# Performance work log

Measured on AMD Instinct MI355X. Metric: run time of the kernel, lower is better.

Reference implementation:

```python
import jax, jax.numpy as jnp
import numpy as np

E = 8       # num_experts
C = 1024    # output_dim (== input_dim, so no input_proj)


def setup_inputs() -> dict:
    key = jax.random.key(0)
    ks = jax.random.split(key, 8)
    B, N = 4, 2048
    s = 0.02
    return {
        "x":    jax.random.normal(ks[0], (B, N, C), jnp.float32),
        "x_ir": jax.random.normal(ks[1], (B, N, C), jnp.float32),
        # expert Linear weights, torch layout (out, in) per expert -> (E, C, C)
        "We": jax.random.normal(ks[2], (E, C, C), jnp.float32) * s,
        "be": jax.random.normal(ks[3], (E, C), jnp.float32) * s,
        # gate: Linear(C, C//2) -> ReLU -> Linear(C//2, E)
        "gw1": jax.random.normal(ks[4], (C // 2, C), jnp.float32) * s,
        "gb1": jax.random.normal(ks[5], (C // 2,), jnp.float32) * s,
        "gw2": jax.random.normal(ks[6], (E, C // 2), jnp.float32) * s,
        "gb2": jax.random.normal(ks[7], (E,), jnp.float32) * s,
    }


def _gates(x, gw1, gb1, gw2, gb2):
    gx = x.mean(axis=1)                                   # [B, C]
    h = jax.nn.relu(gx @ gw1.T + gb1)                     # [B, C//2]
    return jax.nn.softmax(h @ gw2.T + gb2, axis=-1)       # [B, E]


def _moe(x, We, be, g):
    # Equivalent to sum_e g[b,e] * (x @ We[e].T + be[e]); since experts are
    # linear, fold gates into a per-batch weight matrix (compute-efficient).
    Wb = jnp.einsum("be,eoc->boc", g, We)                 # [B, O, C]
    bb = g @ be                                           # [B, O]
    return jnp.einsum("bnc,boc->bno", x, Wb) + bb[:, None, :]


def reference(x, x_ir, We, be, gw1, gb1, gw2, gb2):
    g = _gates(x, gw1, gb1, gw2, gb2)                     # gates computed from x only
    moe_x = _moe(x, We, be, g)
    moe_x_ir = _moe(x_ir, We, be, g)
    return (moe_x, moe_x_ir)
```

## Files before the change

kernel.cpp:

```cpp
#include <hip/hip_runtime.h>
#include <hip/hip_bf16.h>
#include <stdint.h>

#define B_  4
#define N_  2048
#define C_  1024
#define E_  8
#define H_  512

typedef __bf16 bf16x8 __attribute__((ext_vector_type(8)));
typedef __bf16 bf16x4 __attribute__((ext_vector_type(4)));
typedef float  f32x4  __attribute__((ext_vector_type(4)));

#define WB_OFF   0ull
#define PM_OFF   0ull
#define XB_OFF   (8ull*1024*1024)
#define GX_OFF   (XB_OFF + 32ull*1024*1024)
#define BB_OFF   (GX_OFF + 16384ull)
#define H_OFF    (BB_OFF + 16384ull)

__device__ __forceinline__ void gload16(const void* g, void* l) {
  __builtin_amdgcn_global_load_lds((const __attribute__((address_space(1))) void*)g,
                                   (__attribute__((address_space(3))) void*)l, 16, 0, 0);
}

#define CFENCE() asm volatile("" ::: "memory")

__global__ __launch_bounds__(256) void castmean_kernel(const float* __restrict__ x,
    const float* __restrict__ x_ir, __bf16* __restrict__ dst, float* __restrict__ pmean) {
  __shared__ float red[128][9];
  int bi = blockIdx.x;
  int half = bi >> 10, rblk = bi & 1023;
  const float* src = half ? x_ir : x;
  int t = threadIdx.x;
  int cg = t & 127, rg = t >> 7;
  int r0 = rblk * 8 + rg * 4;
  const float4* sp = (const float4*)(src + (size_t)r0 * C_) + cg * 2;
  __bf16* dp = dst + (size_t)half * ((size_t)B_ * N_ * C_) + (size_t)r0 * C_ + cg * 8;
  float s[8] = {};
  #pragma unroll
  for (int rr = 0; rr < 4; ++rr) {
    float4 a = sp[0], b4 = sp[1];
    bf16x8 o;
    o[0] = (__bf16)a.x; o[1] = (__bf16)a.y; o[2] = (__bf16)a.z; o[3] = (__bf16)a.w;
    o[4] = (__bf16)b4.x; o[5] = (__bf16)b4.y; o[6] = (__bf16)b4.z; o[7] = (__bf16)b4.w;
    *(bf16x8*)dp = o;
    s[0] += a.x; s[1] += a.y; s[2] += a.z; s[3] += a.w;
    s[4] += b4.x; s[5] += b4.y; s[6] += b4.z; s[7] += b4.w;
    sp += C_ / 4; dp += C_;
  }
  if (half == 0) {
    if (rg == 1) {
      #pragma unroll
      for (int j = 0; j < 8; ++j) red[cg][j] = s[j];
    }
    __syncthreads();
    if (rg == 0) {
      float4 lo, hi;
      lo.x = s[0] + red[cg][0]; lo.y = s[1] + red[cg][1];
      lo.z = s[2] + red[cg][2]; lo.w = s[3] + red[cg][3];
      hi.x = s[4] + red[cg][4]; hi.y = s[5] + red[cg][5];
      hi.z = s[6] + red[cg][6]; hi.w = s[7] + red[cg][7];
      float* pr = pmean + (size_t)rblk * C_ + cg * 8;
      *(float4*)pr = lo;
      *(float4*)(pr + 4) = hi;
    }
  }
}

__global__ __launch_bounds__(256) void mean2_kernel(const float* __restrict__ pmean,
                                                    float* __restrict__ gx) {
  __shared__ float red[128];
  int cs = blockIdx.x, b = blockIdx.y;
  int t = threadIdx.x;
  int c = cs * 128 + (t & 127), rh = t >> 7;
  const float* p = pmean + ((size_t)b * 256 + rh * 128) * C_ + c;
  float s = 0.f;
  #pragma unroll 8
  for (int j = 0; j < 128; ++j) s += p[(size_t)j * C_];
  if (rh == 1) red[t & 127] = s;
  __syncthreads();
  if (rh == 0) gx[b * C_ + c] = (s + red[t & 127]) * (1.0f / N_);
}

__global__ __launch_bounds__(256) void h_kernel(const float* __restrict__ gx,
    const float* __restrict__ gw1, const float* __restrict__ gb1, float* __restrict__ h) {
  __shared__ float sgx[B_][C_];
  int t = threadIdx.x;
  for (int i = t; i < B_ * C_; i += 256) sgx[i >> 10][i & 1023] = gx[i];
  __syncthreads();
  int jl = t >> 4, l16 = t & 15, b = l16 & 3, qt = l16 >> 2;
  int j = blockIdx.x * 16 + jl;
  const float4* row = (const float4*)(gw1 + (size_t)j * C_) + qt * 64;
  const float* gbase = &sgx[b][qt * 256];
  float acc = 0.f;
  #pragma unroll 8
  for (int c4 = 0; c4 < 64; ++c4) {
    float4 w = row[c4];
    acc += w.x * gbase[c4*4+0] + w.y * gbase[c4*4+1]
         + w.z * gbase[c4*4+2] + w.w * gbase[c4*4+3];
  }
  acc += __shfl_down(acc, 4, 16);
  acc += __shfl_down(acc, 8, 16);
  if (qt == 0) h[b * H_ + j] = fmaxf(acc + gb1[j], 0.f);
}

__global__ __launch_bounds__(256) void wbgate_kernel(const float* __restrict__ h,
    const float* __restrict__ gw2, const float* __restrict__ gb2,
    const float* __restrict__ be, const float* __restrict__ We,
    __bf16* __restrict__ Wb, float* __restrict__ bbp) {
  __shared__ float slog[B_ * E_];
  __shared__ float sg[B_ * E_];
  int t = threadIdx.x;
  int p = t >> 3, sub = t & 7;
  int pb = p >> 3, pe = p & 7;
  float s = 0.f;
  for (int k = sub; k < H_; k += 8) s += h[pb * H_ + k] * gw2[pe * H_ + k];
  s += __shfl_down(s, 4, 8);
  s += __shfl_down(s, 2, 8);
  s += __shfl_down(s, 1, 8);
  if (sub == 0) slog[p] = s + gb2[pe];
  __syncthreads();
  if (t < B_) {
    float m = -1e30f;
    for (int e = 0; e < E_; ++e) m = fmaxf(m, slog[t * E_ + e]);
    float pr[E_], sum = 0.f;
    for (int e = 0; e < E_; ++e) { pr[e] = __expf(slog[t * E_ + e] - m); sum += pr[e]; }
    float inv = 1.f / sum;
    for (int e = 0; e < E_; ++e) sg[t * E_ + e] = pr[e] * inv;
  }
  __syncthreads();

  int bi = blockIdx.x;
  size_t oc4 = (size_t)bi * 256 + t;
  const float4* src = (const float4*)We + oc4;
  float4 w[E_];
  #pragma unroll
  for (int e = 0; e < E_; ++e) w[e] = src[(size_t)e * (C_ * C_ / 4)];
  #pragma unroll
  for (int b = 0; b < B_; ++b) {
    float4 acc = make_float4(0.f, 0.f, 0.f, 0.f);
    #pragma unroll
    for (int e = 0; e < E_; ++e) {
      float g = sg[b * E_ + e];
      acc.x += g * w[e].x; acc.y += g * w[e].y;
      acc.z += g * w[e].z; acc.w += g * w[e].w;
    }
    bf16x4 o;
    o[0] = (__bf16)acc.x; o[1] = (__bf16)acc.y;
    o[2] = (__bf16)acc.z; o[3] = (__bf16)acc.w;
    *(bf16x4*)(Wb + ((size_t)b << 20) + oc4 * 4) = o;
  }

  if (bi < 16) {
    int ii = bi * 256 + t;
    int bb_ = ii >> 10, oo = ii & 1023;
    float sbb = 0.f;
    #pragma unroll
    for (int e = 0; e < E_; ++e) sbb += sg[bb_ * E_ + e] * be[e * C_ + oo];
    bbp[ii] = sbb;
  }
}

#define NT 16

__global__ __launch_bounds__(512, 2) void moe_gemm(const __bf16* __restrict__ Xb,
    const __bf16* __restrict__ Wb, const float* __restrict__ bb, float* __restrict__ out) {
  __shared__ __attribute__((aligned(128))) char smem[2][65536];

  const int t = threadIdx.x;
  const int wid = t >> 6, lane = t & 63;
  const int wm = wid >> 2, wn = wid & 3;

  int f = blockIdx.x;
  int swz = (f & 7) * 32 + (f >> 3);
  int xb_ = swz & 3, yb_ = (swz >> 2) & 7, z = swz >> 5;
  int b = z & 3;
  const size_t mat = (size_t)N_ * C_;
  const __bf16* A  = Xb + (size_t)z * mat;
  const __bf16* Bm = Wb + (size_t)b * C_ * C_;
  float* O = out + (size_t)z * mat;
  const int row0 = yb_ * 256, col0 = xb_ * 256;

  const int lrow8 = lane >> 3;
  const int kblk  = ((lane & 7) ^ lrow8) << 3;

  const int lr = lane & 15;
  const int swzk0 = (((lane >> 4) + 0) ^ (lane & 7)) << 4;
  const int swzk1 = (((lane >> 4) + 4) ^ (lane & 7)) << 4;

  auto stage = [&](int sid, int k0, char* buf) {
    #pragma unroll
    for (int j = 0; j < 2; ++j) {
      int u = wid * 2 + j;
      int rl0 = u * 8;
      if (sid == 0 || sid == 3) {
        int hh = (sid == 3) ? 1 : 0;
        int row_u = rl0 + (rl0 & 64) + hh * 64;
        const __bf16* src = A + (size_t)(row0 + row_u + lrow8) * C_ + k0 + kblk;
        gload16(src, buf + row_u * 128);
      } else {
        int hh = (sid == 2) ? 1 : 0;
        int col_u = (rl0 & 31) + (rl0 >> 5) * 64 + hh * 32;
        const __bf16* src = Bm + (size_t)(col0 + col_u + lrow8) * C_ + k0 + kblk;
        gload16(src, buf + 32768 + col_u * 128);
      }
    }
  };

  f32x4 acc[8][4] = {};
  bf16x8 av[2][4][2];
  bf16x8 bv[2][2][2];

  #define RD_A(buf_, Aq_, mq_) { \
    int rby = (wm * 128 + (Aq_) * 64 + (mq_) * 16 + lr) * 128; \
    av[buf_][mq_][0] = *(const bf16x8*)(rbA + rby + swzk0); \
    av[buf_][mq_][1] = *(const bf16x8*)(rbA + rby + swzk1); }
  #define RD_B(Bq_, nq_) { \
    int cby = (wn * 64 + (Bq_) * 32 + (nq_) * 16 + lr) * 128; \
    bv[Bq_][nq_][0] = *(const bf16x8*)(rbB + cby + swzk0); \
    bv[Bq_][nq_][1] = *(const bf16x8*)(rbB + cby + swzk1); }
  #define MFMA1(ab_, mq_, Bq_, nq_) { \
    acc[(ab_)*4+(mq_)][(Bq_)*2+(nq_)] = __builtin_amdgcn_mfma_f32_16x16x32_bf16( \
        av[ab_][mq_][0], bv[Bq_][nq_][0], acc[(ab_)*4+(mq_)][(Bq_)*2+(nq_)], 0, 0, 0); \
    acc[(ab_)*4+(mq_)][(Bq_)*2+(nq_)] = __builtin_amdgcn_mfma_f32_16x16x32_bf16( \
        av[ab_][mq_][1], bv[Bq_][nq_][1], acc[(ab_)*4+(mq_)][(Bq_)*2+(nq_)], 0, 0, 0); }

  #pragma unroll
  for (int sid = 0; sid < 4; ++sid) stage(sid, 0, smem[0]);
  asm volatile("s_waitcnt vmcnt(2)" ::: "memory");
  __builtin_amdgcn_s_barrier();
  CFENCE();

  for (int kt = 0; kt < NT; ++kt) {
    const char* rbA = smem[kt & 1];
    const char* rbB = rbA + 32768;
    char* wbuf = smem[(kt + 1) & 1];
    const bool more = (kt + 1 < NT);
    const int knext = (kt + 1) * 64;

    if (more) { stage(0, knext, wbuf); stage(1, knext, wbuf); }
    RD_A(0, 0, 0) RD_B(0, 0) RD_A(0, 0, 1) RD_B(0, 1) RD_A(0, 0, 2) RD_A(0, 0, 3)
    __builtin_amdgcn_s_setprio(1);
    MFMA1(0, 0, 0, 0) MFMA1(0, 0, 0, 1)
    RD_B(1, 0) RD_B(1, 1)
    MFMA1(0, 1, 0, 0) MFMA1(0, 1, 0, 1)
    MFMA1(0, 2, 0, 0) MFMA1(0, 2, 0, 1)
    MFMA1(0, 3, 0, 0) MFMA1(0, 3, 0, 1)
    __builtin_amdgcn_s_setprio(0);
    if (more) asm volatile("s_waitcnt vmcnt(4)" ::: "memory");
    else      asm volatile("s_waitcnt vmcnt(0)" ::: "memory");
    __builtin_amdgcn_s_barrier();
    CFENCE();

    if (more) { stage(2, knext, wbuf); stage(3, knext, wbuf); }
    __builtin_amdgcn_s_setprio(1);
    MFMA1(0, 0, 1, 0) MFMA1(0, 0, 1, 1)
    RD_A(1, 1, 0) RD_A(1, 1, 1)
    MFMA1(0, 1, 1, 0) MFMA1(0, 1, 1, 1)
    RD_A(1, 1, 2) RD_A(1, 1, 3)
    MFMA1(0, 2, 1, 0) MFMA1(0, 2, 1, 1)
    MFMA1(0, 3, 1, 0) MFMA1(0, 3, 1, 1)
    __builtin_amdgcn_s_setprio(0);
    __builtin_amdgcn_s_barrier();
    CFENCE();

    __builtin_amdgcn_s_setprio(1);
    MFMA1(1, 0, 0, 0) MFMA1(1, 0, 0, 1) MFMA1(1, 1, 0, 0) MFMA1(1, 1, 0, 1)
    MFMA1(1, 2, 0, 0) MFMA1(1, 2, 0, 1) MFMA1(1, 3, 0, 0) MFMA1(1, 3, 0, 1)
    MFMA1(1, 0, 1, 0) MFMA1(1, 0, 1, 1) MFMA1(1, 1, 1, 0) MFMA1(1, 1, 1, 1)
    MFMA1(1, 2, 1, 0) MFMA1(1, 2, 1, 1) MFMA1(1, 3, 1, 0) MFMA1(1, 3, 1, 1)
    __builtin_amdgcn_s_setprio(0);
    if (more) asm volatile("s_waitcnt vmcnt(2)" ::: "memory");
    __builtin_amdgcn_s_barrier();
    CFENCE();
  }

  const int er = lane >> 4;
  const f32x4 bias4 = *(const f32x4*)(bb + b * C_ + col0 + wn * 64 + lr * 4);

  #pragma unroll
  for (int m = 0; m < 8; ++m) {
    float* eb = (float*)(smem[m & 1]) + wid * (16 * 68);
    #pragma unroll
    for (int n = 0; n < 4; ++n) {
      f32x4 v = acc[m][n];
      #pragma unroll
      for (int r = 0; r < 4; ++r)
        eb[(er * 4 + r) * 68 + n * 16 + lr] = v[r];
    }
    asm volatile("s_waitcnt lgkmcnt(0)" ::: "memory");
    __builtin_amdgcn_sched_barrier(0);
    #pragma unroll
    for (int j = 0; j < 4; ++j) {
      int row = j * 4 + er;
      f32x4 v = *(const f32x4*)(eb + row * 68 + lr * 4);
      v[0] += bias4[0]; v[1] += bias4[1]; v[2] += bias4[2]; v[3] += bias4[3];
      int grow = row0 + wm * 128 + m * 16 + row;
      int gcol = col0 + wn * 64 + lr * 4;
      __builtin_nontemporal_store(v, (f32x4*)(O + (size_t)grow * C_ + gcol));
    }
  }
}

extern "C" void kernel_launch(void* const* d_in, const int* in_sizes, int n_in,
                              void* d_out, int out_size, void* d_ws, size_t ws_size,
                              hipStream_t stream) {
  const float* x    = (const float*)d_in[0];
  const float* x_ir = (const float*)d_in[1];
  const float* We   = (const float*)d_in[2];
  const float* be   = (const float*)d_in[3];
  const float* gw1  = (const float*)d_in[4];
  const float* gb1  = (const float*)d_in[5];
  const float* gw2  = (const float*)d_in[6];
  const float* gb2  = (const float*)d_in[7];
  float* out = (float*)d_out;

  char* ws = (char*)d_ws;
  __bf16* Wb    = (__bf16*)(ws + WB_OFF);
  float*  pmean = (float*)(ws + PM_OFF);
  __bf16* Xb    = (__bf16*)(ws + XB_OFF);
  float*  gx    = (float*)(ws + GX_OFF);
  float*  bbp   = (float*)(ws + BB_OFF);
  float*  h     = (float*)(ws + H_OFF);

  castmean_kernel<<<2048, 256, 0, stream>>>(x, x_ir, Xb, pmean);
  mean2_kernel<<<dim3(8, 4), 256, 0, stream>>>(pmean, gx);
  h_kernel<<<32, 256, 0, stream>>>(gx, gw1, gb1, h);
  wbgate_kernel<<<1024, 256, 0, stream>>>(h, gw2, gb2, be, We, Wb, bbp);

  moe_gemm<<<256, 512, 0, stream>>>(Xb, Wb, bbp, out);
}
```

Before: 92.13 us.

## Prefetch next k-tile LDS fragments during last MFMA phase; nontemporal loads in cast

The GEMM main loop is restructured so the A/B register fragments for the next k-tile are read from LDS during the final MFMA phase of the current tile, after the barrier that makes the next buffer visible. A prologue loads the first tile's fragments before the loop. This aims to hide LDS read latency behind MFMA issue at the start of each iteration. The cast/mean kernel also switches its fp32 input reads to nontemporal loads to reduce cache pollution. The reordering raises register pressure and depends on the barrier and waitcnt placement staying correct for the double buffer.

```diff
diff --git a/kernel.cpp b/kernel.cpp
--- a/kernel.cpp
+++ b/kernel.cpp
@@ -35,18 +35,19 @@
   int t = threadIdx.x;
   int cg = t & 127, rg = t >> 7;
   int r0 = rblk * 8 + rg * 4;
-  const float4* sp = (const float4*)(src + (size_t)r0 * C_) + cg * 2;
+  const f32x4* sp = (const f32x4*)(src + (size_t)r0 * C_) + cg * 2;
   __bf16* dp = dst + (size_t)half * ((size_t)B_ * N_ * C_) + (size_t)r0 * C_ + cg * 8;
   float s[8] = {};
   #pragma unroll
   for (int rr = 0; rr < 4; ++rr) {
-    float4 a = sp[0], b4 = sp[1];
+    f32x4 a  = __builtin_nontemporal_load(sp);
+    f32x4 b4 = __builtin_nontemporal_load(sp + 1);
     bf16x8 o;
-    o[0] = (__bf16)a.x; o[1] = (__bf16)a.y; o[2] = (__bf16)a.z; o[3] = (__bf16)a.w;
-    o[4] = (__bf16)b4.x; o[5] = (__bf16)b4.y; o[6] = (__bf16)b4.z; o[7] = (__bf16)b4.w;
+    o[0] = (__bf16)a[0]; o[1] = (__bf16)a[1]; o[2] = (__bf16)a[2]; o[3] = (__bf16)a[3];
+    o[4] = (__bf16)b4[0]; o[5] = (__bf16)b4[1]; o[6] = (__bf16)b4[2]; o[7] = (__bf16)b4[3];
     *(bf16x8*)dp = o;
-    s[0] += a.x; s[1] += a.y; s[2] += a.z; s[3] += a.w;
-    s[4] += b4.x; s[5] += b4.y; s[6] += b4.z; s[7] += b4.w;
+    s[0] += a[0]; s[1] += a[1]; s[2] += a[2]; s[3] += a[3];
+    s[4] += b4[0]; s[5] += b4[1]; s[6] += b4[2]; s[7] += b4[3];
     sp += C_ / 4; dp += C_;
   }
   if (half == 0) {
@@ -212,41 +213,43 @@
   bf16x8 av[2][4][2];
   bf16x8 bv[2][2][2];
 
-  #define RD_A(buf_, Aq_, mq_) { \
+  #define RD_A(base_, slot_, Aq_, mq_) { \
+    const char* _pA = (base_); \
     int rby = (wm * 128 + (Aq_) * 64 + (mq_) * 16 + lr) * 128; \
-    av[buf_][mq_][0] = *(const bf16x8*)(rbA + rby + swzk0); \
-    av[buf_][mq_][1] = *(const bf16x8*)(rbA + rby + swzk1); }
-  #define RD_B(Bq_, nq_) { \
+    av[slot_][mq_][0] = *(const bf16x8*)(_pA + rby + swzk0); \
+    av[slot_][mq_][1] = *(const bf16x8*)(_pA + rby + swzk1); }
+  #define RD_B(base_, Bq_, nq_) { \
+    const char* _pB = (base_) + 32768; \
     int cby = (wn * 64 + (Bq_) * 32 + (nq_) * 16 + lr) * 128; \
-    bv[Bq_][nq_][0] = *(const bf16x8*)(rbB + cby + swzk0); \
-    bv[Bq_][nq_][1] = *(const bf16x8*)(rbB + cby + swzk1); }
-  #define MFMA1(ab_, mq_, Bq_, nq_) { \
-    acc[(ab_)*4+(mq_)][(Bq_)*2+(nq_)] = __builtin_amdgcn_mfma_f32_16x16x32_bf16( \
-        av[ab_][mq_][0], bv[Bq_][nq_][0], acc[(ab_)*4+(mq_)][(Bq_)*2+(nq_)], 0, 0, 0); \
-    acc[(ab_)*4+(mq_)][(Bq_)*2+(nq_)] = __builtin_amdgcn_mfma_f32_16x16x32_bf16( \
-        av[ab_][mq_][1], bv[Bq_][nq_][1], acc[(ab_)*4+(mq_)][(Bq_)*2+(nq_)], 0, 0, 0); }
+    bv[Bq_][nq_][0] = *(const bf16x8*)(_pB + cby + swzk0); \
+    bv[Bq_][nq_][1] = *(const bf16x8*)(_pB + cby + swzk1); }
+  #define MFMA1(slot_, mq_, Bq_, nq_) { \
+    acc[(slot_)*4+(mq_)][(Bq_)*2+(nq_)] = __builtin_amdgcn_mfma_f32_16x16x32_bf16( \
+        av[slot_][mq_][0], bv[Bq_][nq_][0], acc[(slot_)*4+(mq_)][(Bq_)*2+(nq_)], 0, 0, 0); \
+    acc[(slot_)*4+(mq_)][(Bq_)*2+(nq_)] = __builtin_amdgcn_mfma_f32_16x16x32_bf16( \
+        av[slot_][mq_][1], bv[Bq_][nq_][1], acc[(slot_)*4+(mq_)][(Bq_)*2+(nq_)], 0, 0, 0); }
 
   #pragma unroll
   for (int sid = 0; sid < 4; ++sid) stage(sid, 0, smem[0]);
   asm volatile("s_waitcnt vmcnt(2)" ::: "memory");
   __builtin_amdgcn_s_barrier();
   CFENCE();
+  {
+    const char* rb0 = smem[0];
+    RD_A(rb0, 0, 0, 0) RD_A(rb0, 0, 0, 1) RD_A(rb0, 0, 0, 2) RD_A(rb0, 0, 0, 3)
+    RD_B(rb0, 0, 0) RD_B(rb0, 0, 1) RD_B(rb0, 1, 0) RD_B(rb0, 1, 1)
+  }
 
   for (int kt = 0; kt < NT; ++kt) {
     const char* rbA = smem[kt & 1];
-    const char* rbB = rbA + 32768;
     char* wbuf = smem[(kt + 1) & 1];
     const bool more = (kt + 1 < NT);
     const int knext = (kt + 1) * 64;
 
     if (more) { stage(0, knext, wbuf); stage(1, knext, wbuf); }
-    RD_A(0, 0, 0) RD_B(0, 0) RD_A(0, 0, 1) RD_B(0, 1) RD_A(0, 0, 2) RD_A(0, 0, 3)
     __builtin_amdgcn_s_setprio(1);
-    MFMA1(0, 0, 0, 0) MFMA1(0, 0, 0, 1)
-    RD_B(1, 0) RD_B(1, 1)
-    MFMA1(0, 1, 0, 0) MFMA1(0, 1, 0, 1)
-    MFMA1(0, 2, 0, 0) MFMA1(0, 2, 0, 1)
-    MFMA1(0, 3, 0, 0) MFMA1(0, 3, 0, 1)
+    MFMA1(0, 0, 0, 0) MFMA1(0, 0, 0, 1) MFMA1(0, 1, 0, 0) MFMA1(0, 1, 0, 1)
+    MFMA1(0, 2, 0, 0) MFMA1(0, 2, 0, 1) MFMA1(0, 3, 0, 0) MFMA1(0, 3, 0, 1)
     __builtin_amdgcn_s_setprio(0);
     if (more) asm volatile("s_waitcnt vmcnt(4)" ::: "memory");
     else      asm volatile("s_waitcnt vmcnt(0)" ::: "memory");
@@ -256,24 +259,29 @@
     if (more) { stage(2, knext, wbuf); stage(3, knext, wbuf); }
     __builtin_amdgcn_s_setprio(1);
     MFMA1(0, 0, 1, 0) MFMA1(0, 0, 1, 1)
-    RD_A(1, 1, 0) RD_A(1, 1, 1)
+    RD_A(rbA, 1, 1, 0) RD_A(rbA, 1, 1, 1)
     MFMA1(0, 1, 1, 0) MFMA1(0, 1, 1, 1)
-    RD_A(1, 1, 2) RD_A(1, 1, 3)
+    RD_A(rbA, 1, 1, 2) RD_A(rbA, 1, 1, 3)
     MFMA1(0, 2, 1, 0) MFMA1(0, 2, 1, 1)
     MFMA1(0, 3, 1, 0) MFMA1(0, 3, 1, 1)
     __builtin_amdgcn_s_setprio(0);
     __builtin_amdgcn_s_barrier();
     CFENCE();
 
-    __builtin_amdgcn_s_setprio(1);
-    MFMA1(1, 0, 0, 0) MFMA1(1, 0, 0, 1) MFMA1(1, 1, 0, 0) MFMA1(1, 1, 0, 1)
-    MFMA1(1, 2, 0, 0) MFMA1(1, 2, 0, 1) MFMA1(1, 3, 0, 0) MFMA1(1, 3, 0, 1)
-    MFMA1(1, 0, 1, 0) MFMA1(1, 0, 1, 1) MFMA1(1, 1, 1, 0) MFMA1(1, 1, 1, 1)
-    MFMA1(1, 2, 1, 0) MFMA1(1, 2, 1, 1) MFMA1(1, 3, 1, 0) MFMA1(1, 3, 1, 1)
-    __builtin_amdgcn_s_setprio(0);
     if (more) asm volatile("s_waitcnt vmcnt(2)" ::: "memory");
     __builtin_amdgcn_s_barrier();
     CFENCE();
+    if (more) { RD_A(wbuf, 0, 0, 0) RD_A(wbuf, 0, 0, 1) RD_A(wbuf, 0, 0, 2) RD_A(wbuf, 0, 0, 3) }
+    __builtin_amdgcn_s_setprio(1);
+    MFMA1(1, 0, 0, 0) MFMA1(1, 1, 0, 0) MFMA1(1, 2, 0, 0) MFMA1(1, 3, 0, 0)
+    MFMA1(1, 0, 0, 1) MFMA1(1, 1, 0, 1) MFMA1(1, 2, 0, 1) MFMA1(1, 3, 0, 1)
+    __builtin_amdgcn_s_setprio(0);
+    if (more) { RD_B(wbuf, 0, 0) RD_B(wbuf, 0, 1) }
+    __builtin_amdgcn_s_setprio(1);
+    MFMA1(1, 0, 1, 0) MFMA1(1, 1, 1, 0) MFMA1(1, 2, 1, 0) MFMA1(1, 3, 1, 0)
+    MFMA1(1, 0, 1, 1) MFMA1(1, 1, 1, 1) MFMA1(1, 2, 1, 1) MFMA1(1, 3, 1, 1)
+    __builtin_amdgcn_s_setprio(0);
+    if (more) { RD_B(wbuf, 1, 0) RD_B(wbuf, 1, 1) }
   }
 
   const int er = lane >> 4;
```

New measurement: 95.83 us. 1.04x slower.
